# Optimization experiments

Hardware: AMD Instinct MI355X
Metric: run time of the kernel (lower is better)

## Reference

```python
import jax, jax.numpy as jnp
import numpy as np

B, D, I, H, K = 1024, 128, 64, 256, 8
HE = 2 * H  # encoder cell width (mu || log_sigma2)


def setup_inputs() -> dict:
    key = jax.random.key(0)
    ks = jax.random.split(key, 20)
    g = lambda i, shape, s=0.05: jax.random.normal(ks[i], shape, dtype=jnp.float32) * s
    return dict(
        X=g(0, (B, D, I), 1.0),
        W=jax.random.randint(ks[1], (B, D, I), 0, 2).astype(jnp.int32),
        noise=g(2, (B, H), 1.0),
        A=g(3, (D, I)),  # imputation template (learned)
        enc_Wx=g(4, (I, 4 * HE)), enc_Wh=g(5, (HE, 4 * HE)), enc_b=jnp.zeros((4 * HE,), jnp.float32),
        enc_pi=g(6, (HE,)), enc_pf=g(7, (HE,)), enc_po=g(8, (HE,)),
        dec_Wx=g(9, (I, 4 * H)), dec_Wh=g(10, (H, 4 * H)), dec_b=jnp.zeros((4 * H,), jnp.float32),
        dec_pi=g(11, (H,)), dec_pf=g(12, (H,)), dec_po=g(13, (H,)),
        out_w=g(14, (H, I)), out_b=jnp.full((I,), 0.1, jnp.float32),
        mu_c_unscaled=g(15, (K, H)), sigma2_c_unscaled=g(16, (K, H)), phi_c_unscaled=g(17, (K,)),
    )


def peephole_lstm(x_seq, Wx, Wh, b, pi, pf, po, h0, c0):
    """Keras PeepholeLSTMCell, gate order i,f,c,o. x_seq: [T,B,I] -> (hs [T,B,n], hT, cT)."""
    def step(carry, x):
        h, c = carry
        z = x @ Wx + h @ Wh + b
        zi, zf, zc, zo = jnp.split(z, 4, axis=-1)
        i = jax.nn.sigmoid(zi + pi * c)
        f = jax.nn.sigmoid(zf + pf * c)
        c_new = f * c + i * jnp.tanh(zc)
        o = jax.nn.sigmoid(zo + po * c_new)
        h_new = o * jnp.tanh(c_new)
        return (h_new, c_new), h_new
    (hT, cT), hs = jax.lax.scan(step, (h0, c0), x_seq)
    return hs, hT, cT


def reference(X, W, noise, A, enc_Wx, enc_Wh, enc_b, enc_pi, enc_pf, enc_po,
              dec_Wx, dec_Wh, dec_b, dec_pi, dec_pf, dec_po,
              out_w, out_b, mu_c_unscaled, sigma2_c_unscaled, phi_c_unscaled):
    Bn = X.shape[0]
    Wf = W.astype(X.dtype)
    X_imp = X * Wf + A * (1.0 - Wf)  # masked imputation
    # --- encode: peephole LSTM, take FINAL CELL STATE (encoder_rnn(...)[-1]) ---
    x_seq = jnp.swapaxes(X_imp, 0, 1)  # [D,B,I]
    h0 = jnp.zeros((Bn, HE), X.dtype)
    _, _, cT = peephole_lstm(x_seq, enc_Wx, enc_Wh, enc_b, enc_pi, enc_pf, enc_po, h0, h0)
    mu_tilde = cT[:, :H]
    log_sigma2_tilde = cT[:, H:]
    z = mu_tilde + jnp.exp(0.5 * log_sigma2_tilde) * noise
    # --- decode: zero inputs, initial_state = (h=0, c=z) ---
    dec_in = jnp.zeros((D, Bn, I), X.dtype)
    hs, _, _ = peephole_lstm(dec_in, dec_Wx, dec_Wh, dec_b, dec_pi, dec_pf, dec_po,
                             jnp.zeros((Bn, H), X.dtype), z)
    rnn_out = jnp.swapaxes(hs, 0, 1)  # [B,D,H]
    x_raw = rnn_out @ out_w + out_b   # [B,D,I]
    x = jax.nn.sigmoid(x_raw)
    # --- GMM parameters ---
    mu_c = mu_c_unscaled
    sigma2_c = jax.nn.softplus(sigma2_c_unscaled)
    phi_c = jax.nn.softmax(phi_c_unscaled)
    return (x, x_raw, mu_c, sigma2_c, phi_c, z, mu_tilde, log_sigma2_tilde)
```

## Files before the change

kernel.cpp:

```cpp
#include <hip/hip_runtime.h>
#include <hip/hip_bf16.h>

typedef __attribute__((ext_vector_type(4))) float f32x4;
typedef __attribute__((ext_vector_type(8))) short bf16x8;

#define NB 1024
#define ND 128
#define NI 64
#define NH 256
#define NHE 512
#define KENC 576
#define NENC 2048
#define KDEC 256
#define ESTR 584
#define DSTR 264

__device__ __forceinline__ float sigmf(float x) { return 1.0f / (1.0f + __expf(-x)); }
__device__ __forceinline__ float tanh_f(float x) { return 1.0f - 2.0f / (__expf(2.0f * x) + 1.0f); }

__device__ __forceinline__ f32x4 mfma16(bf16x8 a, bf16x8 b, f32x4 c) {
    return __builtin_amdgcn_mfma_f32_16x16x32_bf16(a, b, c, 0, 0, 0);
}

__device__ __forceinline__ void st_ull(unsigned long long* p, unsigned long long v) {
    __hip_atomic_store(p, v, __ATOMIC_RELAXED, __HIP_MEMORY_SCOPE_AGENT);
}
__device__ __forceinline__ unsigned long long ld_ull(const unsigned long long* p) {
    return __hip_atomic_load(p, __ATOMIC_RELAXED, __HIP_MEMORY_SCOPE_AGENT);
}

__device__ __forceinline__ void spin_ge(const int* p, int target) {
    int g = 0;
    while (__hip_atomic_load(p, __ATOMIC_RELAXED, __HIP_MEMORY_SCOPE_AGENT) < target) {
        __builtin_amdgcn_s_sleep(2);
        if (++g > (1 << 20)) break;
    }
}

__device__ __forceinline__ void quadtr(f32x4 a, int lane,
                                       float& z0, float& z1, float& z2, float& z3) {
    float x0 = a[0], x1 = a[1], x2 = a[2], x3 = a[3];
    float s0 = __shfl_xor(x0, 1), s1 = __shfl_xor(x1, 1),
          s2 = __shfl_xor(x2, 1), s3 = __shfl_xor(x3, 1);
    bool o1 = (lane & 1) != 0;
    float y0 = o1 ? s1 : x0;
    float y1 = o1 ? x1 : s0;
    float y2 = o1 ? s3 : x2;
    float y3 = o1 ? x3 : s2;
    float t0 = __shfl_xor(y0, 2), t1 = __shfl_xor(y1, 2),
          t2 = __shfl_xor(y2, 2), t3 = __shfl_xor(y3, 2);
    bool o2 = (lane & 2) != 0;
    z0 = o2 ? t2 : y0;
    z1 = o2 ? t3 : y1;
    z2 = o2 ? y2 : t0;
    z3 = o2 ? y3 : t1;
}


__global__ void pack_enc_kernel(const float* __restrict__ Wx, const float* __restrict__ Wh,
                                const float* __restrict__ bsrc,
                                __hip_bfloat16* __restrict__ Wp, float* __restrict__ bp)
{
    int n = blockIdx.y;
    int k = blockIdx.x * 256 + threadIdx.x;
    int j = n >> 2, g = n & 3;
    int col = g * NHE + j;
    if (k < KENC) {
        float v = (k < NI) ? Wx[k * NENC + col] : Wh[(k - NI) * NENC + col];
        Wp[(size_t)n * KENC + k] = __float2bfloat16(v);
    }
    if (blockIdx.x == 0 && threadIdx.x == 0) bp[n] = bsrc[col];
}

__global__ void pack_dec_kernel(const float* __restrict__ Wh, const float* __restrict__ ow,
                                const float* __restrict__ bsrc,
                                __hip_bfloat16* __restrict__ Wp, float* __restrict__ bp)
{
    int n = blockIdx.y;
    int k = threadIdx.x;
    float v;
    if (n < 1024) {
        int j = n >> 2, g = n & 3;
        int col = g * NH + j;
        v = Wh[k * 1024 + col];
        if (k == 0) bp[n] = bsrc[col];
    } else if (n < 1088) {
        v = ow[k * NI + (n - 1024)];
    } else {
        v = 0.0f;
    }
    Wp[(size_t)n * KDEC + k] = __float2bfloat16(v);
}

__global__ void pack_xb_kernel(const float* __restrict__ X, const int* __restrict__ W,
                               const float* __restrict__ A, __hip_bfloat16* __restrict__ Xb)
{
    int idx = blockIdx.x * 256 + threadIdx.x;
    int i = idx & 63;
    int t1 = idx >> 6;
    int b = t1 & 1023;
    int d = t1 >> 10;
    int src = (b * ND + d) * NI + i;
    float v = W[src] ? X[src] : A[d * NI + i];
    Xb[idx] = __float2bfloat16(v);
}

__global__ __launch_bounds__(256, 2) void enc_persist(
    const __hip_bfloat16* __restrict__ Xb,
    __hip_bfloat16* __restrict__ h0buf, __hip_bfloat16* __restrict__ h1buf,
    float* __restrict__ cenc,
    const __hip_bfloat16* __restrict__ Wp, const float* __restrict__ bp,
    const float* __restrict__ pi, const float* __restrict__ pf, const float* __restrict__ po,
    int* __restrict__ wrflag)
{
    __shared__ __align__(16) unsigned short Alds[32][ESTR];
    __shared__ __align__(16) unsigned short Hlds[32][36];

    const int tid  = threadIdx.x;
    const int lane = tid & 63;
    const int wv   = tid >> 6;
    const int bm   = blockIdx.x;
    const int bn   = blockIdx.y;
    const int m0   = bm * 32;
    const int lr   = lane & 15;
    const int q    = lane >> 4;
    const int lk   = q * 8;

    bf16x8 breg[2][18];
    #pragma unroll
    for (int ni = 0; ni < 2; ++ni) {
        const __hip_bfloat16* wb = Wp + (size_t)(bn * 128 + wv * 32 + ni * 16 + lr) * KENC + lk;
        #pragma unroll
        for (int i = 0; i < 18; ++i)
            breg[ni][i] = *reinterpret_cast<const bf16x8*>(wb + i * 32);
    }

    const int u = lr >> 2;
    const int e = lane & 3;
    float4 bb[2];
    float ppi[2], ppf[2], ppo[2];
    int jl[2];
    #pragma unroll
    for (int ni = 0; ni < 2; ++ni) {
        jl[ni] = wv * 8 + ni * 4 + u;
        int jg = bn * 32 + jl[ni];
        bb[ni] = *reinterpret_cast<const float4*>(bp + 4 * jg);
        ppi[ni] = pi[jg]; ppf[ni] = pf[jg]; ppo[ni] = po[jg];
    }
    const int rowb = 4 * q + e;

    float creg[2][2] = {{0.f, 0.f}, {0.f, 0.f}};
    __hip_bfloat16* hbuf[2] = {h0buf, h1buf};

    for (int t = 0; t < ND; ++t) {
        {
            int row = tid >> 3, ch = tid & 7;
            *reinterpret_cast<bf16x8*>(&Alds[row][ch * 8]) =
                *reinterpret_cast<const bf16x8*>(Xb + ((size_t)t * NB + m0 + row) * NI + ch * 8);
        }
        if (t > 0 && tid == 0) spin_ge(&wrflag[bm * ND + (t - 1)], 16);
        __syncthreads();

        {
            const unsigned long long* hsrc =
                (const unsigned long long*)(hbuf[t & 1] + (size_t)m0 * NHE);
            #pragma unroll
            for (int it = 0; it < 16; ++it) {
                int idx = tid + it * 256;
                int row = idx >> 7, c8 = idx & 127;
                unsigned long long v = ld_ull(hsrc + (size_t)row * 128 + c8);
                *reinterpret_cast<unsigned long long*>(&Alds[row][64 + c8 * 4]) = v;
            }
        }
        __syncthreads();

        f32x4 acc[2][2];
        #pragma unroll
        for (int mi = 0; mi < 2; ++mi)
            #pragma unroll
            for (int ni = 0; ni < 2; ++ni) acc[mi][ni] = {0.f, 0.f, 0.f, 0.f};
        #pragma unroll
        for (int i = 0; i < 18; ++i) {
            bf16x8 a[2];
            #pragma unroll
            for (int mi = 0; mi < 2; ++mi)
                a[mi] = *reinterpret_cast<const bf16x8*>(&Alds[16 * mi + lr][i * 32 + lk]);
            #pragma unroll
            for (int mi = 0; mi < 2; ++mi)
                #pragma unroll
                for (int ni = 0; ni < 2; ++ni)
                    acc[mi][ni] = mfma16(a[mi], breg[ni][i], acc[mi][ni]);
        }

        #pragma unroll
        for (int mi = 0; mi < 2; ++mi) {
            #pragma unroll
            for (int ni = 0; ni < 2; ++ni) {
                float z0, z1, z2, z3;
                quadtr(acc[mi][ni], lane, z0, z1, z2, z3);
                float c_old = creg[mi][ni];
                float gi = sigmf(z0 + bb[ni].x + ppi[ni] * c_old);
                float gf = sigmf(z1 + bb[ni].y + ppf[ni] * c_old);
                float cn = gf * c_old + gi * tanh_f(z2 + bb[ni].z);
                float go = sigmf(z3 + bb[ni].w + ppo[ni] * cn);
                creg[mi][ni] = cn;
                int row = 16 * mi + rowb;
                __hip_bfloat16 hv = __float2bfloat16(go * tanh_f(cn));
                Hlds[row][jl[ni]] = reinterpret_cast<unsigned short&>(hv);
                if (t == ND - 1)
                    cenc[(size_t)(m0 + row) * NHE + bn * 32 + jl[ni]] = cn;
            }
        }
        __syncthreads();

        if (t < ND - 1) {
            {
                int row = tid >> 3, k8 = tid & 7;
                __hip_bfloat16* hdst = hbuf[(t + 1) & 1];
                unsigned long long v =
                    *reinterpret_cast<const unsigned long long*>(&Hlds[row][k8 * 4]);
                st_ull((unsigned long long*)(hdst + (size_t)(m0 + row) * NHE + bn * 32 + k8 * 4), v);
            }
            __syncthreads();
            if (tid == 0)
                __hip_atomic_fetch_add(&wrflag[bm * ND + t], 1,
                                       __ATOMIC_RELAXED, __HIP_MEMORY_SCOPE_AGENT);
        }
    }
}

__global__ __launch_bounds__(256, 2) void dec_persist(
    __hip_bfloat16* __restrict__ hd0, __hip_bfloat16* __restrict__ hd1,
    const float* __restrict__ zdec,
    const __hip_bfloat16* __restrict__ Wp, const float* __restrict__ bp,
    const float* __restrict__ pi, const float* __restrict__ pf, const float* __restrict__ po,
    const float* __restrict__ ob,
    float* __restrict__ ox, float* __restrict__ oxr,
    int* __restrict__ wr2, int* __restrict__ prd)
{
    __shared__ __align__(16) unsigned short Alds[32][DSTR];
    __shared__ __align__(16) unsigned short Hlds[32][36];

    const int tid  = threadIdx.x;
    const int lane = tid & 63;
    const int wv   = tid >> 6;
    const int bm   = blockIdx.x;
    const int bn   = blockIdx.y;
    const int m0   = bm * 32;
    const int lr   = lane & 15;
    const int q    = lane >> 4;
    const int lk   = q * 8;

    __hip_bfloat16* hbuf[2] = {hd0, hd1};

    if (bn < 8) {
        bf16x8 breg[2][8];
        #pragma unroll
        for (int ni = 0; ni < 2; ++ni) {
            const __hip_bfloat16* wb = Wp + (size_t)(bn * 128 + wv * 32 + ni * 16 + lr) * KDEC + lk;
            #pragma unroll
            for (int i = 0; i < 8; ++i)
                breg[ni][i] = *reinterpret_cast<const bf16x8*>(wb + i * 32);
        }

        const int u = lr >> 2;
        const int e = lane & 3;
        float4 bb[2];
        float ppi[2], ppf[2], ppo[2];
        int jl[2];
        #pragma unroll
        for (int ni = 0; ni < 2; ++ni) {
            jl[ni] = wv * 8 + ni * 4 + u;
            int jg = bn * 32 + jl[ni];
            bb[ni] = *reinterpret_cast<const float4*>(bp + 4 * jg);
            ppi[ni] = pi[jg]; ppf[ni] = pf[jg]; ppo[ni] = po[jg];
        }
        const int rowb = 4 * q + e;

        float creg[2][2];
        #pragma unroll
        for (int mi = 0; mi < 2; ++mi)
            #pragma unroll
            for (int ni = 0; ni < 2; ++ni)
                creg[mi][ni] = zdec[(size_t)(m0 + 16 * mi + rowb) * NH + bn * 32 + jl[ni]];

        for (int t = 0; t < ND; ++t) {
            if (tid == 0) {
                if (t >= 1) spin_ge(&wr2[bm * ND + (t - 1)], 8);
                if (t >= 2) spin_ge(&prd[bm * ND + (t - 2)], 1);
            }
            __syncthreads();

            {
                const unsigned long long* hsrc =
                    (const unsigned long long*)(hbuf[t & 1] + (size_t)m0 * NH);
                #pragma unroll
                for (int it = 0; it < 8; ++it) {
                    int idx = tid + it * 256;
                    int row = idx >> 6, c8 = idx & 63;
                    unsigned long long v = ld_ull(hsrc + (size_t)row * 64 + c8);
                    *reinterpret_cast<unsigned long long*>(&Alds[row][c8 * 4]) = v;
                }
            }
            __syncthreads();

            f32x4 acc[2][2];
            #pragma unroll
            for (int mi = 0; mi < 2; ++mi)
                #pragma unroll
                for (int ni = 0; ni < 2; ++ni) acc[mi][ni] = {0.f, 0.f, 0.f, 0.f};
            #pragma unroll
            for (int i = 0; i < 8; ++i) {
                bf16x8 a[2];
                #pragma unroll
                for (int mi = 0; mi < 2; ++mi)
                    a[mi] = *reinterpret_cast<const bf16x8*>(&Alds[16 * mi + lr][i * 32 + lk]);
                #pragma unroll
                for (int mi = 0; mi < 2; ++mi)
                    #pragma unroll
                    for (int ni = 0; ni < 2; ++ni)
                        acc[mi][ni] = mfma16(a[mi], breg[ni][i], acc[mi][ni]);
            }

            #pragma unroll
            for (int mi = 0; mi < 2; ++mi) {
                #pragma unroll
                for (int ni = 0; ni < 2; ++ni) {
                    float z0, z1, z2, z3;
                    quadtr(acc[mi][ni], lane, z0, z1, z2, z3);
                    float c_old = creg[mi][ni];
                    float gi = sigmf(z0 + bb[ni].x + ppi[ni] * c_old);
                    float gf = sigmf(z1 + bb[ni].y + ppf[ni] * c_old);
                    float cn = gf * c_old + gi * tanh_f(z2 + bb[ni].z);
                    float go = sigmf(z3 + bb[ni].w + ppo[ni] * cn);
                    creg[mi][ni] = cn;
                    int row = 16 * mi + rowb;
                    __hip_bfloat16 hv = __float2bfloat16(go * tanh_f(cn));
                    Hlds[row][jl[ni]] = reinterpret_cast<unsigned short&>(hv);
                }
            }
            __syncthreads();

            {
                int row = tid >> 3, k8 = tid & 7;
                __hip_bfloat16* hdst = hbuf[(t + 1) & 1];
                unsigned long long v =
                    *reinterpret_cast<const unsigned long long*>(&Hlds[row][k8 * 4]);
                st_ull((unsigned long long*)(hdst + (size_t)(m0 + row) * NH + bn * 32 + k8 * 4), v);
            }
            __syncthreads();
            if (tid == 0)
                __hip_atomic_fetch_add(&wr2[bm * ND + t], 1,
                                       __ATOMIC_RELAXED, __HIP_MEMORY_SCOPE_AGENT);
        }
    } else {
        bf16x8 breg[8];
        const __hip_bfloat16* wb = Wp + (size_t)(1024 + wv * 16 + lr) * KDEC + lk;
        #pragma unroll
        for (int i = 0; i < 8; ++i)
            breg[i] = *reinterpret_cast<const bf16x8*>(wb + i * 32);
        const float obv = ob[wv * 16 + lr];

        for (int s = 0; s < ND; ++s) {
            if (tid == 0) spin_ge(&wr2[bm * ND + s], 8);
            __syncthreads();

            {
                const unsigned long long* hsrc =
                    (const unsigned long long*)(hbuf[(s + 1) & 1] + (size_t)m0 * NH);
                #pragma unroll
                for (int it = 0; it < 8; ++it) {
                    int idx = tid + it * 256;
                    int row = idx >> 6, c8 = idx & 63;
                    unsigned long long v = ld_ull(hsrc + (size_t)row * 64 + c8);
                    *reinterpret_cast<unsigned long long*>(&Alds[row][c8 * 4]) = v;
                }
            }
            __syncthreads();
            if (tid == 0)
                __hip_atomic_fetch_add(&prd[bm * ND + s], 1,
                                       __ATOMIC_RELAXED, __HIP_MEMORY_SCOPE_AGENT);

            f32x4 acc[2];
            #pragma unroll
            for (int mi = 0; mi < 2; ++mi) acc[mi] = {0.f, 0.f, 0.f, 0.f};
            #pragma unroll
            for (int i = 0; i < 8; ++i) {
                bf16x8 a[2];
                #pragma unroll
                for (int mi = 0; mi < 2; ++mi)
                    a[mi] = *reinterpret_cast<const bf16x8*>(&Alds[16 * mi + lr][i * 32 + lk]);
                #pragma unroll
                for (int mi = 0; mi < 2; ++mi)
                    acc[mi] = mfma16(a[mi], breg[i], acc[mi]);
            }

            int colp = wv * 16 + lr;
            #pragma unroll
            for (int mi = 0; mi < 2; ++mi) {
                #pragma unroll
                for (int v = 0; v < 4; ++v) {
                    int row = m0 + 16 * mi + 4 * q + v;
                    float val = acc[mi][v] + obv;
                    size_t off = (size_t)row * (ND * NI) + (size_t)s * NI + colp;
                    oxr[off] = val;
                    ox[off]  = sigmf(val);
                }
            }
        }
    }
}

__global__ void mid_kernel(const float* __restrict__ cenc, const float* __restrict__ noise,
                           float* __restrict__ zdec, float* __restrict__ oz,
                           float* __restrict__ omut, float* __restrict__ olst)
{
    int idx = blockIdx.x * 256 + threadIdx.x;
    int b = idx >> 8, h = idx & 255;
    float mu = cenc[b * NHE + h];
    float ls = cenc[b * NHE + NH + h];
    float zz = mu + expf(0.5f * ls) * noise[idx];
    omut[idx] = mu;
    olst[idx] = ls;
    oz[idx]   = zz;
    zdec[idx] = zz;
}

__global__ void mix_kernel(const float* __restrict__ mu_in, const float* __restrict__ s2_in,
                           const float* __restrict__ phi_in,
                           float* __restrict__ mu_out, float* __restrict__ s2_out,
                           float* __restrict__ phi_out)
{
    int idx = blockIdx.x * 256 + threadIdx.x;
    mu_out[idx] = mu_in[idx];
    float x = s2_in[idx];
    s2_out[idx] = (x > 20.0f) ? x : log1pf(expf(x));
    if (idx == 0) {
        float m = phi_in[0];
        for (int k = 1; k < 8; ++k) m = fmaxf(m, phi_in[k]);
        float e[8], s = 0.0f;
        for (int k = 0; k < 8; ++k) { e[k] = expf(phi_in[k] - m); s += e[k]; }
        for (int k = 0; k < 8; ++k) phi_out[k] = e[k] / s;
    }
}

extern "C" void kernel_launch(void* const* d_in, const int* in_sizes, int n_in,
                              void* d_out, int out_size, void* d_ws, size_t ws_size,
                              hipStream_t stream)
{
    const float* X     = (const float*)d_in[0];
    const int*   W     = (const int*)d_in[1];
    const float* noise = (const float*)d_in[2];
    const float* A     = (const float*)d_in[3];
    const float* eWx   = (const float*)d_in[4];
    const float* eWh   = (const float*)d_in[5];
    const float* eb    = (const float*)d_in[6];
    const float* epi   = (const float*)d_in[7];
    const float* epf   = (const float*)d_in[8];
    const float* epo   = (const float*)d_in[9];
    const float* dWh   = (const float*)d_in[11];
    const float* db    = (const float*)d_in[12];
    const float* dpi   = (const float*)d_in[13];
    const float* dpf   = (const float*)d_in[14];
    const float* dpo   = (const float*)d_in[15];
    const float* ow    = (const float*)d_in[16];
    const float* ob    = (const float*)d_in[17];
    const float* muc   = (const float*)d_in[18];
    const float* s2c   = (const float*)d_in[19];
    const float* phic  = (const float*)d_in[20];

    float* out = (float*)d_out;
    float* o_x    = out;
    float* o_xraw = out + 8388608;
    float* o_muc  = out + 16777216;
    float* o_s2c  = out + 16779264;
    float* o_phic = out + 16781312;
    float* o_z    = out + 16781320;
    float* o_mut  = out + 17043464;
    float* o_lst  = out + 17305608;

    char* ws = (char*)d_ws;
    __hip_bfloat16* Wencp = (__hip_bfloat16*)(ws + 0);
    __hip_bfloat16* Wdecp = (__hip_bfloat16*)(ws + 2359296);
    float*          bencp = (float*)(ws + 2949120);
    float*          bdecp = (float*)(ws + 2957312);
    __hip_bfloat16* Xb    = (__hip_bfloat16*)(ws + 2965504);
    __hip_bfloat16* he0   = (__hip_bfloat16*)(ws + 19742720);
    __hip_bfloat16* he1   = (__hip_bfloat16*)(ws + 20791296);
    float*          cenc  = (float*)(ws + 21839872);
    __hip_bfloat16* hd0   = (__hip_bfloat16*)(ws + 23937024);
    __hip_bfloat16* hd1   = (__hip_bfloat16*)(ws + 24461312);
    float*          zdec  = (float*)(ws + 24985600);
    int*            encwr = (int*)(ws + 26034176);
    int*            decwr = (int*)(ws + 26050560);
    int*            decpr = (int*)(ws + 26066944);

    hipMemsetAsync(he0, 0, 1048576, stream);
    hipMemsetAsync(hd0, 0, 524288, stream);
    hipMemsetAsync(encwr, 0, 49152, stream);

    pack_enc_kernel<<<dim3(3, 2048), 256, 0, stream>>>(eWx, eWh, eb, Wencp, bencp);
    pack_dec_kernel<<<dim3(1, 1152), 256, 0, stream>>>(dWh, ow, db, Wdecp, bdecp);
    pack_xb_kernel<<<32768, 256, 0, stream>>>(X, W, A, Xb);

    enc_persist<<<dim3(32, 16), 256, 0, stream>>>(
        Xb, he0, he1, cenc, Wencp, bencp, epi, epf, epo, encwr);

    mid_kernel<<<1024, 256, 0, stream>>>(cenc, noise, zdec, o_z, o_mut, o_lst);
    mix_kernel<<<8, 256, 0, stream>>>(muc, s2c, phic, o_muc, o_s2c, o_phic);

    dec_persist<<<dim3(32, 9), 256, 0, stream>>>(
        hd0, hd1, zdec, Wdecp, bdecp, dpi, dpf, dpo, ob, o_x, o_xraw, decwr, decpr);
}
```

Baseline: 1.728 ms.

## Replace atomic counters with per-producer flags and overlap input GEMM with spin wait

Cross-block step synchronisation moves from one fetch-add counter per step to a flag slot per producer block. The wait is now done by every wave, with each lane polling one flag and a wavefront vote deciding when all are set, which removes the tid==0 spin plus __syncthreads handoff. In the encoder, the MFMA work on the x-input part (first two K slices) is issued before waiting on the previous hidden state, so it overlaps with the wait. The flag arrays are larger, so more memory is cleared per launch, and every wave now issues polling loads.

```diff
diff --git a/kernel.cpp b/kernel.cpp
--- a/kernel.cpp
+++ b/kernel.cpp
@@ -28,12 +28,21 @@
 __device__ __forceinline__ unsigned long long ld_ull(const unsigned long long* p) {
     return __hip_atomic_load(p, __ATOMIC_RELAXED, __HIP_MEMORY_SCOPE_AGENT);
 }
-
-__device__ __forceinline__ void spin_ge(const int* p, int target) {
+__device__ __forceinline__ void st_flag(int* p) {
+    __hip_atomic_store(p, 1, __ATOMIC_RELAXED, __HIP_MEMORY_SCOPE_AGENT);
+}
+
+__device__ __forceinline__ void wspin(const int* flags, int n, int lane, const int* extra) {
     int g = 0;
-    while (__hip_atomic_load(p, __ATOMIC_RELAXED, __HIP_MEMORY_SCOPE_AGENT) < target) {
-        __builtin_amdgcn_s_sleep(2);
-        if (++g > (1 << 20)) break;
+    for (;;) {
+        int v = 1;
+        if (lane < n)
+            v = __hip_atomic_load(flags + lane, __ATOMIC_RELAXED, __HIP_MEMORY_SCOPE_AGENT);
+        else if (extra != nullptr && lane == n)
+            v = __hip_atomic_load(extra, __ATOMIC_RELAXED, __HIP_MEMORY_SCOPE_AGENT);
+        if (__all(v != 0)) return;
+        __builtin_amdgcn_s_sleep(1);
+        if (++g > (1 << 20)) return;
     }
 }
 
@@ -111,7 +120,7 @@
     float* __restrict__ cenc,
     const __hip_bfloat16* __restrict__ Wp, const float* __restrict__ bp,
     const float* __restrict__ pi, const float* __restrict__ pf, const float* __restrict__ po,
-    int* __restrict__ wrflag)
+    int* __restrict__ encfl)
 {
     __shared__ __align__(16) unsigned short Alds[32][ESTR];
     __shared__ __align__(16) unsigned short Hlds[32][36];
@@ -158,8 +167,27 @@
             *reinterpret_cast<bf16x8*>(&Alds[row][ch * 8]) =
                 *reinterpret_cast<const bf16x8*>(Xb + ((size_t)t * NB + m0 + row) * NI + ch * 8);
         }
-        if (t > 0 && tid == 0) spin_ge(&wrflag[bm * ND + (t - 1)], 16);
         __syncthreads();
+
+        f32x4 acc[2][2];
+        #pragma unroll
+        for (int mi = 0; mi < 2; ++mi)
+            #pragma unroll
+            for (int ni = 0; ni < 2; ++ni) acc[mi][ni] = {0.f, 0.f, 0.f, 0.f};
+        #pragma unroll
+        for (int i = 0; i < 2; ++i) {
+            bf16x8 a[2];
+            #pragma unroll
+            for (int mi = 0; mi < 2; ++mi)
+                a[mi] = *reinterpret_cast<const bf16x8*>(&Alds[16 * mi + lr][i * 32 + lk]);
+            #pragma unroll
+            for (int mi = 0; mi < 2; ++mi)
+                #pragma unroll
+                for (int ni = 0; ni < 2; ++ni)
+                    acc[mi][ni] = mfma16(a[mi], breg[ni][i], acc[mi][ni]);
+        }
+
+        if (t > 0) wspin(encfl + (size_t)(bm * ND + (t - 1)) * 16, 16, lane, nullptr);
 
         {
             const unsigned long long* hsrc =
@@ -174,13 +202,8 @@
         }
         __syncthreads();
 
-        f32x4 acc[2][2];
-        #pragma unroll
-        for (int mi = 0; mi < 2; ++mi)
-            #pragma unroll
-            for (int ni = 0; ni < 2; ++ni) acc[mi][ni] = {0.f, 0.f, 0.f, 0.f};
-        #pragma unroll
-        for (int i = 0; i < 18; ++i) {
+        #pragma unroll
+        for (int i = 2; i < 18; ++i) {
             bf16x8 a[2];
             #pragma unroll
             for (int mi = 0; mi < 2; ++mi)
@@ -222,9 +245,7 @@
                 st_ull((unsigned long long*)(hdst + (size_t)(m0 + row) * NHE + bn * 32 + k8 * 4), v);
             }
             __syncthreads();
-            if (tid == 0)
-                __hip_atomic_fetch_add(&wrflag[bm * ND + t], 1,
-                                       __ATOMIC_RELAXED, __HIP_MEMORY_SCOPE_AGENT);
+            if (tid == 0) st_flag(encfl + (size_t)(bm * ND + t) * 16 + bn);
         }
     }
 }
@@ -236,7 +257,7 @@
     const float* __restrict__ pi, const float* __restrict__ pf, const float* __restrict__ po,
     const float* __restrict__ ob,
     float* __restrict__ ox, float* __restrict__ oxr,
-    int* __restrict__ wr2, int* __restrict__ prd)
+    int* __restrict__ decfl, int* __restrict__ decpr)
 {
     __shared__ __align__(16) unsigned short Alds[32][DSTR];
     __shared__ __align__(16) unsigned short Hlds[32][36];
@@ -285,11 +306,10 @@
                 creg[mi][ni] = zdec[(size_t)(m0 + 16 * mi + rowb) * NH + bn * 32 + jl[ni]];
 
         for (int t = 0; t < ND; ++t) {
-            if (tid == 0) {
-                if (t >= 1) spin_ge(&wr2[bm * ND + (t - 1)], 8);
-                if (t >= 2) spin_ge(&prd[bm * ND + (t - 2)], 1);
-            }
-            __syncthreads();
+            if (t >= 1) {
+                const int* ex = (t >= 2) ? (decpr + bm * ND + (t - 2)) : nullptr;
+                wspin(decfl + (size_t)(bm * ND + (t - 1)) * 8, 8, lane, ex);
+            }
 
             {
                 const unsigned long long* hsrc =
@@ -349,9 +369,7 @@
                 st_ull((unsigned long long*)(hdst + (size_t)(m0 + row) * NH + bn * 32 + k8 * 4), v);
             }
             __syncthreads();
-            if (tid == 0)
-                __hip_atomic_fetch_add(&wr2[bm * ND + t], 1,
-                                       __ATOMIC_RELAXED, __HIP_MEMORY_SCOPE_AGENT);
+            if (tid == 0) st_flag(decfl + (size_t)(bm * ND + t) * 8 + bn);
         }
     } else {
         bf16x8 breg[8];
@@ -362,7 +380,7 @@
         const float obv = ob[wv * 16 + lr];
 
         for (int s = 0; s < ND; ++s) {
-            if (tid == 0) spin_ge(&wr2[bm * ND + s], 8);
+            wspin(decfl + (size_t)(bm * ND + s) * 8, 8, lane, nullptr);
             __syncthreads();
 
             {
@@ -377,9 +395,7 @@
                 }
             }
             __syncthreads();
-            if (tid == 0)
-                __hip_atomic_fetch_add(&prd[bm * ND + s], 1,
-                                       __ATOMIC_RELAXED, __HIP_MEMORY_SCOPE_AGENT);
+            if (tid == 0) st_flag(decpr + bm * ND + s);
 
             f32x4 acc[2];
             #pragma unroll
@@ -491,24 +507,24 @@
     __hip_bfloat16* hd0   = (__hip_bfloat16*)(ws + 23937024);
     __hip_bfloat16* hd1   = (__hip_bfloat16*)(ws + 24461312);
     float*          zdec  = (float*)(ws + 24985600);
-    int*            encwr = (int*)(ws + 26034176);
-    int*            decwr = (int*)(ws + 26050560);
-    int*            decpr = (int*)(ws + 26066944);
+    int*            encfl = (int*)(ws + 26034176);
+    int*            decfl = (int*)(ws + 26296320);
+    int*            decpr = (int*)(ws + 26427392);
 
     hipMemsetAsync(he0, 0, 1048576, stream);
     hipMemsetAsync(hd0, 0, 524288, stream);
-    hipMemsetAsync(encwr, 0, 49152, stream);
+    hipMemsetAsync(encfl, 0, 409600, stream);
 
     pack_enc_kernel<<<dim3(3, 2048), 256, 0, stream>>>(eWx, eWh, eb, Wencp, bencp);
     pack_dec_kernel<<<dim3(1, 1152), 256, 0, stream>>>(dWh, ow, db, Wdecp, bdecp);
     pack_xb_kernel<<<32768, 256, 0, stream>>>(X, W, A, Xb);
 
     enc_persist<<<dim3(32, 16), 256, 0, stream>>>(
-        Xb, he0, he1, cenc, Wencp, bencp, epi, epf, epo, encwr);
+        Xb, he0, he1, cenc, Wencp, bencp, epi, epf, epo, encfl);
 
     mid_kernel<<<1024, 256, 0, stream>>>(cenc, noise, zdec, o_z, o_mut, o_lst);
     mix_kernel<<<8, 256, 0, stream>>>(muc, s2c, phic, o_muc, o_s2c, o_phic);
 
     dec_persist<<<dim3(32, 9), 256, 0, stream>>>(
-        hd0, hd1, zdec, Wdecp, bdecp, dpi, dpf, dpo, ob, o_x, o_xraw, decwr, decpr);
-}
+        hd0, hd1, zdec, Wdecp, bdecp, dpi, dpf, dpo, ob, o_x, o_xraw, decfl, decpr);
+}
```

Measured after the change: 1.703 ms. No clear change (-1.5%).
